# Kernel optimization log

Hardware: AMD Instinct MI355X
Metric: run time of the kernel (lower is better)

The kernel has to match this reference:

```python
import jax, jax.numpy as jnp
import numpy as np

N = 100000   # nodes
E = 1600000  # edges
D = 128      # hidden_dim (also input feature dim)
R = 8        # num_relations
B = 4        # num_bases
OUT = 64     # out_dim
P = 2        # gating exponent p


def setup_inputs() -> dict:
    key = jax.random.key(0)
    ks = jax.random.split(key, 16)
    w = lambda k, shape, s=0.05: jax.random.normal(k, shape, dtype=jnp.float32) * s
    return {
        "x": jax.random.normal(ks[0], (N, D), dtype=jnp.float32),
        "src": jax.random.randint(ks[1], (E,), 0, N, dtype=jnp.int32),
        "dst": jax.random.randint(ks[2], (E,), 0, N, dtype=jnp.int32),
        "edge_type": jax.random.randint(ks[3], (E,), 0, R, dtype=jnp.int32),
        "proj_W": w(ks[4], (D, D)), "proj_b": jnp.zeros((D,), jnp.float32),
        "basis1": w(ks[5], (B, D, D)), "comp1": w(ks[6], (R, B), 1.0),
        "root1": w(ks[7], (D, D)), "bias1": jnp.zeros((D,), jnp.float32),
        "basis2": w(ks[8], (B, D, D)), "comp2": w(ks[9], (R, B), 1.0),
        "root2": w(ks[10], (D, D)), "bias2": jnp.zeros((D,), jnp.float32),
        "out_W": w(ks[11], (D, OUT)), "out_b": jnp.zeros((OUT,), jnp.float32),
    }


def _rgcn(x, src, dst, et, basis, comp, root, bias):
    # PyG RGCNConv (basis decomposition, aggr='mean'):
    # out_i = x_i @ root + bias + sum_r mean_{e: dst=i, type=r}( x_{src_e} @ W_r )
    # Mean is linear, so aggregate raw features per (node, relation), then matmul.
    n, d = x.shape
    seg = dst * R + et                                   # combined (node, relation) key
    agg = jax.ops.segment_sum(x[src], seg, num_segments=n * R).reshape(n, R, d)
    cnt = jax.ops.segment_sum(jnp.ones(seg.shape, x.dtype), seg, num_segments=n * R).reshape(n, R)
    agg = agg / jnp.maximum(cnt, 1.0)[:, :, None]        # empty segments -> 0
    W = jnp.einsum('rb,bdf->rdf', comp, basis)           # [R, D, D] relation weights
    return jnp.einsum('nrd,rdf->nf', agg, W) + x @ root + bias


def _gate(x, src, dst):
    # tau = tanh(scatter_mean(|x_src - x_dst|^p, index=src))
    diff = jnp.abs(x[src] - x[dst]) ** P                 # [E, D]
    s = jax.ops.segment_sum(diff, src, num_segments=x.shape[0])
    c = jax.ops.segment_sum(jnp.ones(src.shape, x.dtype), src, num_segments=x.shape[0])
    return jnp.tanh(s / jnp.maximum(c, 1.0)[:, None])


def reference(x, src, dst, edge_type, proj_W, proj_b,
              basis1, comp1, root1, bias1,
              basis2, comp2, root2, bias2,
              out_W, out_b):
    # input projection (dropout is identity in eval mode)
    h = jax.nn.relu(x @ proj_W + proj_b)
    latents = [h]
    for basis, comp, root, bias in ((basis1, comp1, root1, bias1),
                                    (basis2, comp2, root2, bias2)):
        h_new = jax.nn.relu(_rgcn(h, src, dst, edge_type, basis, comp, root, bias))
        tau = _gate(h, src, dst)
        h = (1.0 - tau) * h + tau * h_new
        latents.append(h)
    out = h @ out_W + out_b
    return (out, jnp.stack(latents))
```

## Files before the change

kernel.cpp:

```cpp
#include <hip/hip_runtime.h>
#include <cstdint>
#include <cstddef>

#define D 128
#define RR 8

typedef __attribute__((ext_vector_type(8))) short short8;
typedef __attribute__((ext_vector_type(4))) float f32x4;

__device__ inline ushort f2b(float x) {
    union { float f; unsigned u; } v; v.f = x;
    unsigned r = v.u + 0x7fff + ((v.u >> 16) & 1);
    return (ushort)(r >> 16);
}
__device__ inline float b2f(ushort u) {
    union { unsigned u; float f; } v; v.u = ((unsigned)u) << 16; return v.f;
}

__device__ inline void gload_lds16(const ushort* g, ushort* l) {
    __builtin_amdgcn_global_load_lds(
        (const __attribute__((address_space(1))) unsigned int*)g,
        (__attribute__((address_space(3))) unsigned int*)l, 16, 0, 0);
}

template<bool BIAS, bool RELU, bool STF, bool STB>
__global__ __launch_bounds__(256, 4) void gemm_bf16(
    const ushort* __restrict__ A0, int lda0, int k0steps,
    const ushort* __restrict__ A1, int lda1,
    const ushort* __restrict__ BT, int ktiles,
    const float* __restrict__ bias, float* __restrict__ Cf, int ldcf,
    ushort* __restrict__ Cb, int ldcb, int M, int ncol)
{
    __shared__ ushort As[128 * 64];
    __shared__ ushort Bs[128 * 64];
    const int tid = threadIdx.x;
    const int m0 = blockIdx.x * 128;
    const int ldb = ktiles * 128;
    const int ksteps = ktiles * 2;

    const int w = tid >> 6, lane = tid & 63;
    const int wm = (w & 1) * 64, wn = (w >> 1) * 64;
    const int l15 = lane & 15, quad = lane >> 4;

    const ushort* a0p[4];
    const ushort* a1p[4];
    const ushort* bp[4];
#pragma unroll
    for (int it = 0; it < 4; it++) {
        int gi = w * 256 + it * 64 + lane;
        int row = gi >> 3, g = gi & 7;
        int cg = g ^ (row & 7);
        int gr = m0 + row; if (gr > M - 1) gr = M - 1;
        a0p[it] = A0 + (size_t)gr * lda0 + (cg << 3);
        a1p[it] = A1 + (size_t)gr * lda1 + (cg << 3);
        bp[it]  = BT + (size_t)row * ldb + (cg << 3);
    }

    f32x4 acc[4][4];
    const f32x4 z4 = {0.f, 0.f, 0.f, 0.f};
#pragma unroll
    for (int i = 0; i < 4; i++)
#pragma unroll
        for (int j = 0; j < 4; j++) acc[i][j] = z4;

    for (int kt = 0; kt < ksteps; kt++) {
        const int ko = kt * 64;
        if (kt < k0steps) {
#pragma unroll
            for (int it = 0; it < 4; it++)
                gload_lds16(a0p[it] + ko, As + w * 2048 + it * 512);
        } else {
            const int ko1 = (kt - k0steps) * 64;
#pragma unroll
            for (int it = 0; it < 4; it++)
                gload_lds16(a1p[it] + ko1, As + w * 2048 + it * 512);
        }
#pragma unroll
        for (int it = 0; it < 4; it++)
            gload_lds16(bp[it] + ko, Bs + w * 2048 + it * 512);
        __syncthreads();

#pragma unroll
        for (int ks = 0; ks < 64; ks += 32) {
            const int q0 = (ks >> 3) + quad;
            short8 af[4], bfr[4];
#pragma unroll
            for (int i = 0; i < 4; i++) {
                int row = wm + i * 16 + l15;
                af[i] = *(const short8*)(&As[row * 64 + ((q0 ^ (row & 7)) << 3)]);
            }
#pragma unroll
            for (int j = 0; j < 4; j++) {
                int row = wn + j * 16 + l15;
                bfr[j] = *(const short8*)(&Bs[row * 64 + ((q0 ^ (row & 7)) << 3)]);
            }
#pragma unroll
            for (int i = 0; i < 4; i++)
#pragma unroll
                for (int j = 0; j < 4; j++)
                    acc[i][j] = __builtin_amdgcn_mfma_f32_16x16x32_bf16(
                        af[i], bfr[j], acc[i][j], 0, 0, 0);
        }
        __syncthreads();
    }

#pragma unroll
    for (int i = 0; i < 4; i++) {
#pragma unroll
        for (int q = 0; q < 4; q++) {
            int gm = m0 + wm + i * 16 + quad * 4 + q;
            if (gm >= M) continue;
#pragma unroll
            for (int j = 0; j < 4; j++) {
                int gn = wn + j * 16 + l15;
                if (gn >= ncol) continue;
                float v = acc[i][j][q];
                if (BIAS) v += bias[gn];
                if (RELU) v = v > 0.f ? v : 0.f;
                if (STF) Cf[(size_t)gm * ldcf + gn] = v;
                if (STB) Cb[(size_t)gm * ldcb + gn] = f2b(v);
            }
        }
    }
}

__global__ void build_bigBT(const float* __restrict__ basis,
                            const float* __restrict__ comp,
                            const float* __restrict__ root,
                            ushort* __restrict__ BT)
{
    int i = blockIdx.x * 256 + threadIdx.x;
    if (i >= 128 * 1152) return;
    int f = i / 1152, c = i - f * 1152;
    float a;
    if (c < 1024) {
        int r = c >> 7, d = c & 127;
        a = 0.f;
#pragma unroll
        for (int b = 0; b < 4; b++)
            a += comp[r * 4 + b] * basis[(b * 128 + d) * 128 + f];
    } else {
        a = root[(c - 1024) * 128 + f];
    }
    BT[i] = f2b(a);
}

__global__ void transpose_pad(const float* __restrict__ in, ushort* __restrict__ out,
                              int cols)
{
    int i = blockIdx.x * 256 + threadIdx.x;
    if (i >= 128 * 128) return;
    int k = i & 127, f = i >> 7;
    out[i] = (f < cols) ? f2b(in[k * cols + f]) : (ushort)0;
}

__global__ void cast_x(const float* __restrict__ in, ushort* __restrict__ Hc, int total4)
{
    int i = blockIdx.x * 256 + threadIdx.x;
    if (i >= total4) return;
    float4 v = ((const float4*)in)[i];
    ushort4 o = { f2b(v.x), f2b(v.y), f2b(v.z), f2b(v.w) };
    *(ushort4*)(Hc + (size_t)i * 4) = o;
}

__global__ void count_slot(const int* __restrict__ src, const int* __restrict__ dst,
                           const int* __restrict__ et, int* __restrict__ cnt,
                           int* __restrict__ deg, int* __restrict__ slotA,
                           int* __restrict__ slotG, int E)
{
    int t = blockIdx.x * 256 + threadIdx.x;
    int e0 = t * 4;
    if (e0 + 4 <= E) {
        int4 s4 = ((const int4*)src)[t];
        int4 d4 = ((const int4*)dst)[t];
        int4 t4 = ((const int4*)et)[t];
        int4 sa, sg;
        sa.x = atomicAdd(&cnt[d4.x * RR + t4.x], 1);
        sa.y = atomicAdd(&cnt[d4.y * RR + t4.y], 1);
        sa.z = atomicAdd(&cnt[d4.z * RR + t4.z], 1);
        sa.w = atomicAdd(&cnt[d4.w * RR + t4.w], 1);
        sg.x = atomicAdd(&deg[s4.x], 1);
        sg.y = atomicAdd(&deg[s4.y], 1);
        sg.z = atomicAdd(&deg[s4.z], 1);
        sg.w = atomicAdd(&deg[s4.w], 1);
        ((int4*)slotA)[t] = sa;
        ((int4*)slotG)[t] = sg;
    } else {
        for (int e = e0; e < E; e++) {
            slotA[e] = atomicAdd(&cnt[dst[e] * RR + et[e]], 1);
            slotG[e] = atomicAdd(&deg[src[e]], 1);
        }
    }
}

__global__ void scan1(const int* __restrict__ in, int* __restrict__ bsum, int n)
{
    __shared__ int s[256];
    const int b = blockIdx.x, t = threadIdx.x;
    const int base = b * 1024;
    int v = 0;
#pragma unroll
    for (int i = 0; i < 4; i++) {
        int idx = base + t * 4 + i;
        if (idx < n) v += in[idx];
    }
    s[t] = v; __syncthreads();
    for (int off = 128; off > 0; off >>= 1) {
        if (t < off) s[t] += s[t + off];
        __syncthreads();
    }
    if (t == 0) bsum[b] = s[0];
}

__global__ void scan_top(int* __restrict__ bsum, int nb)
{
    __shared__ int s[1024];
    const int t = threadIdx.x;
    int v = (t < nb) ? bsum[t] : 0;
    s[t] = v; __syncthreads();
    for (int off = 1; off < 1024; off <<= 1) {
        int x = (t >= off) ? s[t - off] : 0;
        __syncthreads();
        s[t] += x;
        __syncthreads();
    }
    if (t < nb) bsum[t] = s[t] - v;
}

__global__ void scan2(const int* __restrict__ in, const int* __restrict__ bsum,
                      int* __restrict__ out, int n)
{
    __shared__ int s[256];
    const int b = blockIdx.x, t = threadIdx.x;
    const int base = b * 1024;
    int loc[4];
    int v = 0;
#pragma unroll
    for (int i = 0; i < 4; i++) {
        int idx = base + t * 4 + i;
        int x = (idx < n) ? in[idx] : 0;
        loc[i] = v; v += x;
    }
    s[t] = v; __syncthreads();
    for (int off = 1; off < 256; off <<= 1) {
        int x = (t >= off) ? s[t - off] : 0;
        __syncthreads();
        s[t] += x;
        __syncthreads();
    }
    const int add = bsum[b] + (s[t] - v);
#pragma unroll
    for (int i = 0; i < 4; i++) {
        int idx = base + t * 4 + i;
        if (idx < n) out[idx] = add + loc[i];
    }
}

__global__ void fill_scatter(const int* __restrict__ src, const int* __restrict__ dst,
                             const int* __restrict__ et,
                             const int* __restrict__ aoff, const int* __restrict__ goff,
                             const int* __restrict__ slotA, const int* __restrict__ slotG,
                             int* __restrict__ acsr, int* __restrict__ gcsr, int E)
{
    int t = blockIdx.x * 256 + threadIdx.x;
    int e0 = t * 4;
    if (e0 + 4 <= E) {
        int4 s4 = ((const int4*)src)[t];
        int4 d4 = ((const int4*)dst)[t];
        int4 t4 = ((const int4*)et)[t];
        int4 sa = ((const int4*)slotA)[t];
        int4 sg = ((const int4*)slotG)[t];
        acsr[aoff[d4.x * RR + t4.x] + sa.x] = s4.x;
        acsr[aoff[d4.y * RR + t4.y] + sa.y] = s4.y;
        acsr[aoff[d4.z * RR + t4.z] + sa.z] = s4.z;
        acsr[aoff[d4.w * RR + t4.w] + sa.w] = s4.w;
        gcsr[goff[s4.x] + sg.x] = d4.x;
        gcsr[goff[s4.y] + sg.y] = d4.y;
        gcsr[goff[s4.z] + sg.z] = d4.z;
        gcsr[goff[s4.w] + sg.w] = d4.w;
    } else {
        for (int e = e0; e < E; e++) {
            int s0 = src[e], d0 = dst[e];
            acsr[aoff[d0 * RR + et[e]] + slotA[e]] = s0;
            gcsr[goff[s0] + slotG[e]] = d0;
        }
    }
}

__global__ __launch_bounds__(256) void gate_gather(
    const ushort* __restrict__ Hc, const int* __restrict__ gcsr,
    const int* __restrict__ goff, const int* __restrict__ deg,
    ushort* __restrict__ TAUb, int N)
{
    const int g = threadIdx.x >> 4, lane = threadIdx.x & 15;
    const int n = blockIdx.x * 16 + g;
    if (n >= N) return;
    const int start = goff[n];
    const int c = deg[n];
    const ushort* hbase = Hc + lane * 8;
    const short8 a8 = *(const short8*)(hbase + (size_t)n * 128);
    float av[8];
#pragma unroll
    for (int j = 0; j < 8; j++) av[j] = b2f((ushort)a8[j]);
    float acc[8];
#pragma unroll
    for (int j = 0; j < 8; j++) acc[j] = 0.f;

    int i = 0;
    for (; i + 8 <= c; i += 8) {
        int dd[8];
#pragma unroll
        for (int k = 0; k < 8; k++)
            dd[k] = __builtin_nontemporal_load(&gcsr[start + i + k]);
        short8 bb[8];
#pragma unroll
        for (int k = 0; k < 8; k++)
            bb[k] = *(const short8*)(hbase + (size_t)dd[k] * 128);
#pragma unroll
        for (int k = 0; k < 8; k++)
#pragma unroll
            for (int j = 0; j < 8; j++) {
                float dx = av[j] - b2f((ushort)bb[k][j]);
                acc[j] += dx * dx;
            }
    }
    if (i + 4 <= c) {
        int dd[4];
#pragma unroll
        for (int k = 0; k < 4; k++)
            dd[k] = __builtin_nontemporal_load(&gcsr[start + i + k]);
        short8 bb[4];
#pragma unroll
        for (int k = 0; k < 4; k++)
            bb[k] = *(const short8*)(hbase + (size_t)dd[k] * 128);
#pragma unroll
        for (int k = 0; k < 4; k++)
#pragma unroll
            for (int j = 0; j < 8; j++) {
                float dx = av[j] - b2f((ushort)bb[k][j]);
                acc[j] += dx * dx;
            }
        i += 4;
    }
    if (i + 2 <= c) {
        int d0 = __builtin_nontemporal_load(&gcsr[start + i]);
        int d1 = __builtin_nontemporal_load(&gcsr[start + i + 1]);
        short8 b0 = *(const short8*)(hbase + (size_t)d0 * 128);
        short8 b1 = *(const short8*)(hbase + (size_t)d1 * 128);
#pragma unroll
        for (int j = 0; j < 8; j++) {
            float dx0 = av[j] - b2f((ushort)b0[j]);
            float dx1 = av[j] - b2f((ushort)b1[j]);
            acc[j] += dx0 * dx0 + dx1 * dx1;
        }
        i += 2;
    }
    if (i < c) {
        int d0 = __builtin_nontemporal_load(&gcsr[start + i]);
        short8 b0 = *(const short8*)(hbase + (size_t)d0 * 128);
#pragma unroll
        for (int j = 0; j < 8; j++) {
            float dx0 = av[j] - b2f((ushort)b0[j]);
            acc[j] += dx0 * dx0;
        }
    }
    const float inv = (c > 0) ? (1.f / (float)c) : 1.f;
    short8 t;
#pragma unroll
    for (int j = 0; j < 8; j++) t[j] = (short)f2b(tanhf(acc[j] * inv));
    *(short8*)(TAUb + (size_t)n * D + lane * 8) = t;
}

__global__ __launch_bounds__(256) void agg_gather(
    ushort* __restrict__ Agg, const ushort* __restrict__ Hc,
    const int* __restrict__ acsr, const int* __restrict__ aoff,
    const int* __restrict__ cnt, int N)
{
    const int g = threadIdx.x >> 4, lane = threadIdx.x & 15;
    const int n = blockIdx.x * 16 + g;
    if (n >= N) return;
    const int sbase = n * RR;
    const int start = aoff[sbase];
    int ctot = 0;
#pragma unroll
    for (int r0 = 0; r0 < RR; r0++) ctot += cnt[sbase + r0];

    const ushort* hbase = Hc + lane * 8;
    ushort* obase = Agg + (size_t)n * 1024 + lane * 8;

    float cum[8];
#pragma unroll
    for (int j = 0; j < 8; j++) cum[j] = 0.f;
    int r = 0;
    int segstart = 0;
    int nexte = cnt[sbase];

    auto flush = [&]() {
        int c = nexte - segstart;
        short8 outv = {0, 0, 0, 0, 0, 0, 0, 0};
        if (c > 0) {
            float inv = 1.f / (float)c;
#pragma unroll
            for (int j = 0; j < 8; j++) outv[j] = (short)f2b(cum[j] * inv);
        }
        __builtin_nontemporal_store(outv, (short8*)(obase + r * 128));
#pragma unroll
        for (int j = 0; j < 8; j++) cum[j] = 0.f;
        segstart = nexte;
        r++;
        if (r < RR) nexte += cnt[sbase + r];
    };

    int i = 0;
    for (; i + 8 <= ctot; i += 8) {
        int ss[8];
#pragma unroll
        for (int k = 0; k < 8; k++)
            ss[k] = __builtin_nontemporal_load(&acsr[start + i + k]);
        short8 yy[8];
#pragma unroll
        for (int k = 0; k < 8; k++)
            yy[k] = *(const short8*)(hbase + (size_t)ss[k] * 128);
#pragma unroll
        for (int k = 0; k < 8; k++) {
            while (i + k >= nexte) flush();
#pragma unroll
            for (int j = 0; j < 8; j++) cum[j] += b2f((ushort)yy[k][j]);
        }
    }
    for (; i < ctot; i++) {
        int s0 = __builtin_nontemporal_load(&acsr[start + i]);
        short8 y0 = *(const short8*)(hbase + (size_t)s0 * 128);
        while (i >= nexte) flush();
#pragma unroll
        for (int j = 0; j < 8; j++) cum[j] += b2f((ushort)y0[j]);
    }
    while (r < RR) flush();
}

__global__ void finalize(const float* __restrict__ hp, float* __restrict__ hn,
                         const ushort* __restrict__ TAUb, ushort* __restrict__ Hc,
                         int total4)
{
    int idx = blockIdx.x * 256 + threadIdx.x;
    if (idx >= total4) return;
    const float4 p = ((const float4*)hp)[idx];
    const float4 a = ((const float4*)hn)[idx];
    const ushort4 t4 = ((const ushort4*)TAUb)[idx];
    float4 o;
    o.x = p.x + b2f(t4.x) * (a.x - p.x);
    o.y = p.y + b2f(t4.y) * (a.y - p.y);
    o.z = p.z + b2f(t4.z) * (a.z - p.z);
    o.w = p.w + b2f(t4.w) * (a.w - p.w);
    ((float4*)hn)[idx] = o;
    ushort4 ob = { f2b(o.x), f2b(o.y), f2b(o.z), f2b(o.w) };
    *(ushort4*)(Hc + (size_t)idx * 4) = ob;
}

extern "C" void kernel_launch(void* const* d_in, const int* in_sizes, int n_in,
                              void* d_out, int out_size, void* d_ws, size_t ws_size,
                              hipStream_t stream)
{
    const float* x      = (const float*)d_in[0];
    const int*   src    = (const int*)  d_in[1];
    const int*   dst    = (const int*)  d_in[2];
    const int*   etyp   = (const int*)  d_in[3];
    const float* projW  = (const float*)d_in[4];
    const float* projb  = (const float*)d_in[5];
    const float* basis1 = (const float*)d_in[6];
    const float* comp1  = (const float*)d_in[7];
    const float* root1  = (const float*)d_in[8];
    const float* bias1  = (const float*)d_in[9];
    const float* basis2 = (const float*)d_in[10];
    const float* comp2  = (const float*)d_in[11];
    const float* root2  = (const float*)d_in[12];
    const float* bias2  = (const float*)d_in[13];
    const float* outW   = (const float*)d_in[14];
    const float* outb   = (const float*)d_in[15];

    const int N    = in_sizes[0] / D;
    const int E    = in_sizes[1];
    const int OUTD = in_sizes[15];

    float* out  = (float*)d_out;
    float* lat0 = out + (size_t)N * OUTD;
    float* lat1 = lat0 + (size_t)N * D;
    float* lat2 = lat1 + (size_t)N * D;

    char* p = (char*)d_ws;
    ushort* Agg   = (ushort*)p;  p += (size_t)N * 1024 * 2;
    ushort* Hc    = (ushort*)p;  p += (size_t)N * 128 * 2;
    ushort* TAUb  = (ushort*)p;  p += (size_t)N * D * 2;
    ushort* projWT = (ushort*)p; p += 16384 * 2;
    ushort* outWT  = (ushort*)p; p += 16384 * 2;
    ushort* bigBT1 = (ushort*)p; p += (size_t)128 * 1152 * 2;
    ushort* bigBT2 = (ushort*)p; p += (size_t)128 * 1152 * 2;
    int* cnt_i  = (int*)p;       p += (size_t)N * RR * 4;
    int* deg_i  = (int*)p;       p += (size_t)N * 4;
    int* aoff   = (int*)p;       p += (size_t)N * RR * 4;
    int* goff   = (int*)p;       p += (size_t)N * 4;
    int* slotA  = (int*)p;       p += (size_t)E * 4;
    int* slotG  = (int*)p;       p += (size_t)E * 4;
    int* acsr   = (int*)p;       p += (size_t)E * 4;
    int* gcsr   = (int*)p;       p += (size_t)E * 4;
    int* bsum   = (int*)p;       p += 4096;

    if ((size_t)(p - (char*)d_ws) > ws_size) return;

    hipMemsetAsync(cnt_i, 0, sizeof(int) * ((size_t)N * RR + N), stream);

    build_bigBT<<<(128 * 1152 + 255) / 256, 256, 0, stream>>>(basis1, comp1, root1, bigBT1);
    build_bigBT<<<(128 * 1152 + 255) / 256, 256, 0, stream>>>(basis2, comp2, root2, bigBT2);
    transpose_pad<<<64, 256, 0, stream>>>(projW, projWT, 128);
    transpose_pad<<<64, 256, 0, stream>>>(outW, outWT, OUTD);

    cast_x<<<(N * 32 + 255) / 256, 256, 0, stream>>>(x, Hc, N * 32);

    count_slot<<<(E / 4 + 255) / 256, 256, 0, stream>>>(
        src, dst, etyp, cnt_i, deg_i, slotA, slotG, E);

    {
        int n1 = N * RR, nb1 = (n1 + 1023) / 1024;
        scan1<<<nb1, 256, 0, stream>>>(cnt_i, bsum, n1);
        scan_top<<<1, 1024, 0, stream>>>(bsum, nb1);
        scan2<<<nb1, 256, 0, stream>>>(cnt_i, bsum, aoff, n1);
        int nb2 = (N + 1023) / 1024;
        scan1<<<nb2, 256, 0, stream>>>(deg_i, bsum, N);
        scan_top<<<1, 1024, 0, stream>>>(bsum, nb2);
        scan2<<<nb2, 256, 0, stream>>>(deg_i, bsum, goff, N);
    }

    fill_scatter<<<(E / 4 + 255) / 256, 256, 0, stream>>>(
        src, dst, etyp, aoff, goff, slotA, slotG, acsr, gcsr, E);

    const int mb = (N + 127) / 128;
    const int nodeblocks16 = (N + 15) / 16;

    gemm_bf16<true, true, true, true><<<mb, 256, 0, stream>>>(
        Hc, 128, 2, Hc, 128, projWT, 1, projb, lat0, 128, Hc, 128, N, 128);

    const ushort* bigBT[2] = {bigBT1, bigBT2};
    const float* biases[2] = {bias1, bias2};
    float* lats[3]         = {lat0, lat1, lat2};

    for (int l = 0; l < 2; l++) {
        float* hn = lats[l + 1];

        gate_gather<<<nodeblocks16, 256, 0, stream>>>(Hc, gcsr, goff, deg_i, TAUb, N);
        agg_gather<<<nodeblocks16, 256, 0, stream>>>(Agg, Hc, acsr, aoff, cnt_i, N);

        gemm_bf16<true, true, true, false><<<mb, 256, 0, stream>>>(
            Agg, 1024, 16, Hc, 128, bigBT[l], 9, biases[l], hn, 128, nullptr, 0, N, 128);

        finalize<<<(N * 32 + 255) / 256, 256, 0, stream>>>(
            lats[l], hn, TAUb, Hc, N * 32);
    }

    gemm_bf16<true, false, true, false><<<mb, 256, 0, stream>>>(
        Hc, 128, 2, Hc, 128, outWT, 1, outb, out, OUTD, nullptr, 0, N, OUTD);
}
```

Measured before the change: 1.089 ms.

## Fuse per-relation mean aggregation into the RGCN GEMM via LDS tiles

Replaces the separate agg_gather kernel, which wrote an N×8×128 bf16 aggregate buffer, and the following GEMM with one fused kernel. For each relation it gathers and averages neighbor rows directly into an LDS A-tile, then runs MFMA against that relation's weight slice, and finishes with the root term from Hc. This removes the large intermediate write and read of Agg but serializes the gather latency with the MFMA work inside each block and lowers occupancy through the larger LDS footprint. The gate gather loop is also simplified to 4-way unrolling and drops nontemporal index loads.

Result: slower. 1.250 ms (+14.7%).

```diff
diff --git a/kernel.cpp b/kernel.cpp
--- a/kernel.cpp
+++ b/kernel.cpp
@@ -21,6 +21,163 @@
     __builtin_amdgcn_global_load_lds(
         (const __attribute__((address_space(1))) unsigned int*)g,
         (__attribute__((address_space(3))) unsigned int*)l, 16, 0, 0);
+}
+
+__global__ __launch_bounds__(256, 3) void rgcn_fused(
+    const ushort* __restrict__ Hc,
+    const int* __restrict__ acsr, const int* __restrict__ aoff,
+    const int* __restrict__ cnt,
+    const ushort* __restrict__ BT,
+    const float* __restrict__ bias,
+    float* __restrict__ hn, int M)
+{
+    __shared__ ushort As[128 * 128];
+    __shared__ ushort Bs[128 * 64];
+    const int tid = threadIdx.x;
+    const int m0 = blockIdx.x * 128;
+
+    const int w = tid >> 6, lane = tid & 63;
+    const int wm = (w & 1) * 64, wn = (w >> 1) * 64;
+    const int l15 = lane & 15, quad = lane >> 4;
+
+    const ushort* bp[4];
+#pragma unroll
+    for (int it = 0; it < 4; it++) {
+        int gi = w * 256 + it * 64 + lane;
+        int row = gi >> 3, g = gi & 7;
+        int cg = g ^ (row & 7);
+        bp[it] = BT + (size_t)row * 1152 + (cg << 3);
+    }
+    const ushort* hp[8];
+#pragma unroll
+    for (int it = 0; it < 8; it++) {
+        int gi = w * 512 + it * 64 + lane;
+        int row = gi >> 4, g = gi & 15;
+        int cg = g ^ (row & 15);
+        int gr = m0 + row; if (gr > M - 1) gr = M - 1;
+        hp[it] = Hc + (size_t)gr * 128 + (cg << 3);
+    }
+
+    const int gl = tid & 15;
+    const int gn0 = tid >> 4;
+    const ushort* hb = Hc + gl * 8;
+
+    f32x4 acc[4][4];
+    const f32x4 z4 = {0.f, 0.f, 0.f, 0.f};
+#pragma unroll
+    for (int i = 0; i < 4; i++)
+#pragma unroll
+        for (int j = 0; j < 4; j++) acc[i][j] = z4;
+
+    for (int r = 0; r < 9; r++) {
+#pragma unroll
+        for (int it = 0; it < 4; it++)
+            gload_lds16(bp[it] + r * 128, Bs + w * 2048 + it * 512);
+
+        if (r < 8) {
+            for (int pass = 0; pass < 8; pass++) {
+                const int nn = pass * 16 + gn0;
+                int n = m0 + nn; if (n > M - 1) n = M - 1;
+                const int seg = n * RR + r;
+                const int st = aoff[seg];
+                const int c = cnt[seg];
+                float a[8];
+#pragma unroll
+                for (int j = 0; j < 8; j++) a[j] = 0.f;
+                int i = 0;
+                for (; i + 4 <= c; i += 4) {
+                    int s0 = acsr[st + i],     s1 = acsr[st + i + 1];
+                    int s2 = acsr[st + i + 2], s3 = acsr[st + i + 3];
+                    short8 y0 = *(const short8*)(hb + (size_t)s0 * 128);
+                    short8 y1 = *(const short8*)(hb + (size_t)s1 * 128);
+                    short8 y2 = *(const short8*)(hb + (size_t)s2 * 128);
+                    short8 y3 = *(const short8*)(hb + (size_t)s3 * 128);
+#pragma unroll
+                    for (int j = 0; j < 8; j++)
+                        a[j] += (b2f((ushort)y0[j]) + b2f((ushort)y1[j]))
+                              + (b2f((ushort)y2[j]) + b2f((ushort)y3[j]));
+                }
+                if (i + 2 <= c) {
+                    int s0 = acsr[st + i], s1 = acsr[st + i + 1];
+                    short8 y0 = *(const short8*)(hb + (size_t)s0 * 128);
+                    short8 y1 = *(const short8*)(hb + (size_t)s1 * 128);
+#pragma unroll
+                    for (int j = 0; j < 8; j++)
+                        a[j] += b2f((ushort)y0[j]) + b2f((ushort)y1[j]);
+                    i += 2;
+                }
+                if (i < c) {
+                    int s0 = acsr[st + i];
+                    short8 y0 = *(const short8*)(hb + (size_t)s0 * 128);
+#pragma unroll
+                    for (int j = 0; j < 8; j++)
+                        a[j] += b2f((ushort)y0[j]);
+                }
+                short8 outv = {0, 0, 0, 0, 0, 0, 0, 0};
+                if (c > 0) {
+                    float inv = 1.f / (float)c;
+#pragma unroll
+                    for (int j = 0; j < 8; j++) outv[j] = (short)f2b(a[j] * inv);
+                }
+                *(short8*)(&As[nn * 128 + ((gl ^ (nn & 15)) << 3)]) = outv;
+            }
+        } else {
+#pragma unroll
+            for (int it = 0; it < 8; it++)
+                gload_lds16(hp[it], As + w * 4096 + it * 512);
+        }
+        __syncthreads();
+
+#pragma unroll
+        for (int h = 0; h < 2; h++) {
+            if (h == 1) {
+                __syncthreads();
+#pragma unroll
+                for (int it = 0; it < 4; it++)
+                    gload_lds16(bp[it] + r * 128 + 64, Bs + w * 2048 + it * 512);
+                __syncthreads();
+            }
+#pragma unroll
+            for (int s = 0; s < 2; s++) {
+                const int g0a = ((h * 64 + s * 32) >> 3) + quad;
+                const int g0b = ((s * 32) >> 3) + quad;
+                short8 af[4], bfr[4];
+#pragma unroll
+                for (int i = 0; i < 4; i++) {
+                    int row = wm + i * 16 + l15;
+                    af[i] = *(const short8*)(&As[row * 128 + ((g0a ^ (row & 15)) << 3)]);
+                }
+#pragma unroll
+                for (int j = 0; j < 4; j++) {
+                    int row = wn + j * 16 + l15;
+                    bfr[j] = *(const short8*)(&Bs[row * 64 + ((g0b ^ (row & 7)) << 3)]);
+                }
+#pragma unroll
+                for (int i = 0; i < 4; i++)
+#pragma unroll
+                    for (int j = 0; j < 4; j++)
+                        acc[i][j] = __builtin_amdgcn_mfma_f32_16x16x32_bf16(
+                            af[i], bfr[j], acc[i][j], 0, 0, 0);
+            }
+        }
+        __syncthreads();
+    }
+
+#pragma unroll
+    for (int i = 0; i < 4; i++) {
+#pragma unroll
+        for (int q = 0; q < 4; q++) {
+            int gm = m0 + wm + i * 16 + quad * 4 + q;
+            if (gm >= M) continue;
+#pragma unroll
+            for (int j = 0; j < 4; j++) {
+                int gn = wn + j * 16 + l15;
+                float v = acc[i][j][q] + bias[gn];
+                v = v > 0.f ? v : 0.f;
+                hn[(size_t)gm * 128 + gn] = v;
+            }
+        }
+    }
 }
 
 template<bool BIAS, bool RELU, bool STF, bool STB>
@@ -307,44 +464,24 @@
     for (int j = 0; j < 8; j++) acc[j] = 0.f;
 
     int i = 0;
-    for (; i + 8 <= c; i += 8) {
-        int dd[8];
-#pragma unroll
-        for (int k = 0; k < 8; k++)
-            dd[k] = __builtin_nontemporal_load(&gcsr[start + i + k]);
-        short8 bb[8];
-#pragma unroll
-        for (int k = 0; k < 8; k++)
-            bb[k] = *(const short8*)(hbase + (size_t)dd[k] * 128);
-#pragma unroll
-        for (int k = 0; k < 8; k++)
-#pragma unroll
-            for (int j = 0; j < 8; j++) {
-                float dx = av[j] - b2f((ushort)bb[k][j]);
-                acc[j] += dx * dx;
-            }
-    }
-    if (i + 4 <= c) {
-        int dd[4];
-#pragma unroll
-        for (int k = 0; k < 4; k++)
-            dd[k] = __builtin_nontemporal_load(&gcsr[start + i + k]);
-        short8 bb[4];
-#pragma unroll
-        for (int k = 0; k < 4; k++)
-            bb[k] = *(const short8*)(hbase + (size_t)dd[k] * 128);
-#pragma unroll
-        for (int k = 0; k < 4; k++)
-#pragma unroll
-            for (int j = 0; j < 8; j++) {
-                float dx = av[j] - b2f((ushort)bb[k][j]);
-                acc[j] += dx * dx;
-            }
-        i += 4;
+    for (; i + 4 <= c; i += 4) {
+        int d0 = gcsr[start + i],     d1 = gcsr[start + i + 1];
+        int d2 = gcsr[start + i + 2], d3 = gcsr[start + i + 3];
+        short8 b0 = *(const short8*)(hbase + (size_t)d0 * 128);
+        short8 b1 = *(const short8*)(hbase + (size_t)d1 * 128);
+        short8 b2 = *(const short8*)(hbase + (size_t)d2 * 128);
+        short8 b3 = *(const short8*)(hbase + (size_t)d3 * 128);
+#pragma unroll
+        for (int j = 0; j < 8; j++) {
+            float dx0 = av[j] - b2f((ushort)b0[j]);
+            float dx1 = av[j] - b2f((ushort)b1[j]);
+            float dx2 = av[j] - b2f((ushort)b2[j]);
+            float dx3 = av[j] - b2f((ushort)b3[j]);
+            acc[j] += dx0 * dx0 + dx1 * dx1 + dx2 * dx2 + dx3 * dx3;
+        }
     }
     if (i + 2 <= c) {
-        int d0 = __builtin_nontemporal_load(&gcsr[start + i]);
-        int d1 = __builtin_nontemporal_load(&gcsr[start + i + 1]);
+        int d0 = gcsr[start + i], d1 = gcsr[start + i + 1];
         short8 b0 = *(const short8*)(hbase + (size_t)d0 * 128);
         short8 b1 = *(const short8*)(hbase + (size_t)d1 * 128);
 #pragma unroll
@@ -356,7 +493,7 @@
         i += 2;
     }
     if (i < c) {
-        int d0 = __builtin_nontemporal_load(&gcsr[start + i]);
+        int d0 = gcsr[start + i];
         short8 b0 = *(const short8*)(hbase + (size_t)d0 * 128);
 #pragma unroll
         for (int j = 0; j < 8; j++) {
@@ -369,73 +506,6 @@
 #pragma unroll
     for (int j = 0; j < 8; j++) t[j] = (short)f2b(tanhf(acc[j] * inv));
     *(short8*)(TAUb + (size_t)n * D + lane * 8) = t;
-}
-
-__global__ __launch_bounds__(256) void agg_gather(
-    ushort* __restrict__ Agg, const ushort* __restrict__ Hc,
-    const int* __restrict__ acsr, const int* __restrict__ aoff,
-    const int* __restrict__ cnt, int N)
-{
-    const int g = threadIdx.x >> 4, lane = threadIdx.x & 15;
-    const int n = blockIdx.x * 16 + g;
-    if (n >= N) return;
-    const int sbase = n * RR;
-    const int start = aoff[sbase];
-    int ctot = 0;
-#pragma unroll
-    for (int r0 = 0; r0 < RR; r0++) ctot += cnt[sbase + r0];
-
-    const ushort* hbase = Hc + lane * 8;
-    ushort* obase = Agg + (size_t)n * 1024 + lane * 8;
-
-    float cum[8];
-#pragma unroll
-    for (int j = 0; j < 8; j++) cum[j] = 0.f;
-    int r = 0;
-    int segstart = 0;
-    int nexte = cnt[sbase];
-
-    auto flush = [&]() {
-        int c = nexte - segstart;
-        short8 outv = {0, 0, 0, 0, 0, 0, 0, 0};
-        if (c > 0) {
-            float inv = 1.f / (float)c;
-#pragma unroll
-            for (int j = 0; j < 8; j++) outv[j] = (short)f2b(cum[j] * inv);
-        }
-        __builtin_nontemporal_store(outv, (short8*)(obase + r * 128));
-#pragma unroll
-        for (int j = 0; j < 8; j++) cum[j] = 0.f;
-        segstart = nexte;
-        r++;
-        if (r < RR) nexte += cnt[sbase + r];
-    };
-
-    int i = 0;
-    for (; i + 8 <= ctot; i += 8) {
-        int ss[8];
-#pragma unroll
-        for (int k = 0; k < 8; k++)
-            ss[k] = __builtin_nontemporal_load(&acsr[start + i + k]);
-        short8 yy[8];
-#pragma unroll
-        for (int k = 0; k < 8; k++)
-            yy[k] = *(const short8*)(hbase + (size_t)ss[k] * 128);
-#pragma unroll
-        for (int k = 0; k < 8; k++) {
-            while (i + k >= nexte) flush();
-#pragma unroll
-            for (int j = 0; j < 8; j++) cum[j] += b2f((ushort)yy[k][j]);
-        }
-    }
-    for (; i < ctot; i++) {
-        int s0 = __builtin_nontemporal_load(&acsr[start + i]);
-        short8 y0 = *(const short8*)(hbase + (size_t)s0 * 128);
-        while (i >= nexte) flush();
-#pragma unroll
-        for (int j = 0; j < 8; j++) cum[j] += b2f((ushort)y0[j]);
-    }
-    while (r < RR) flush();
 }
 
 __global__ void finalize(const float* __restrict__ hp, float* __restrict__ hn,
@@ -488,7 +558,6 @@
     float* lat2 = lat1 + (size_t)N * D;
 
     char* p = (char*)d_ws;
-    ushort* Agg   = (ushort*)p;  p += (size_t)N * 1024 * 2;
     ushort* Hc    = (ushort*)p;  p += (size_t)N * 128 * 2;
     ushort* TAUb  = (ushort*)p;  p += (size_t)N * D * 2;
     ushort* projWT = (ushort*)p; p += 16384 * 2;
@@ -547,10 +616,9 @@
         float* hn = lats[l + 1];
 
         gate_gather<<<nodeblocks16, 256, 0, stream>>>(Hc, gcsr, goff, deg_i, TAUb, N);
-        agg_gather<<<nodeblocks16, 256, 0, stream>>>(Agg, Hc, acsr, aoff, cnt_i, N);
-
-        gemm_bf16<true, true, true, false><<<mb, 256, 0, stream>>>(
-            Agg, 1024, 16, Hc, 128, bigBT[l], 9, biases[l], hn, 128, nullptr, 0, N, 128);
+
+        rgcn_fused<<<mb, 256, 0, stream>>>(
+            Hc, acsr, aoff, cnt_i, bigBT[l], biases[l], hn, N);
 
         finalize<<<(N * 32 + 255) / 256, 256, 0, stream>>>(
             lats[l], hn, TAUb, Hc, N * 32);
```
